# Performance work log

Hardware: AMD Instinct MI355X
Metric: run time of the kernel (lower is better)

## Reference

```python
import jax, jax.numpy as jnp
import numpy as np
import math

B, T, C = 4, 2048, 1024
N_HEAD = 16
HEAD_DIM = C // N_HEAD


def setup_inputs() -> dict:
    key = jax.random.key(0)
    k1, k2, k3, k4, k5 = jax.random.split(key, 5)
    s = 1.0 / math.sqrt(C)
    return {
        "x": jax.random.normal(k1, (B, T, C), dtype=jnp.float32),
        "W_attn": jax.random.normal(k2, (3 * C, C), dtype=jnp.float32) * s,
        "b_attn": jax.random.normal(k3, (3 * C,), dtype=jnp.float32) * 0.02,
        "W_proj": jax.random.normal(k4, (C, C), dtype=jnp.float32) * s,
        "b_proj": jax.random.normal(k5, (C,), dtype=jnp.float32) * 0.02,
    }


def reference(x, W_attn, b_attn, W_proj, b_proj):
    Bx, Tx, Cx = x.shape
    # QKV projection (torch Linear: x @ W.T + b), split into q,k,v
    qkv = jnp.einsum("btc,dc->btd", x, W_attn) + b_attn  # [B,T,3C]
    q, k, v = jnp.split(qkv, 3, axis=-1)
    # [B,T,C] -> [B,H,T,hd]
    def to_heads(t):
        return t.reshape(Bx, Tx, N_HEAD, HEAD_DIM).transpose(0, 2, 1, 3)
    q, k, v = to_heads(q), to_heads(k), to_heads(v)
    scale = 1.0 / math.sqrt(HEAD_DIM)
    att = jnp.einsum("bhqd,bhkd->bhqk", q, k) * scale  # [B,H,T,T]
    causal = jnp.tril(jnp.ones((Tx, Tx), dtype=bool))
    att = jnp.where(causal, att, -jnp.inf)
    att = jax.nn.softmax(att, axis=-1)
    y = jnp.einsum("bhqk,bhkd->bhqd", att, v)  # [B,H,T,hd]
    y = y.transpose(0, 2, 1, 3).reshape(Bx, Tx, Cx)
    y = jnp.einsum("btc,dc->btd", y, W_proj) + b_proj
    return y
```

## Files before the change

kernel.cpp:

```cpp
#include <hip/hip_runtime.h>
#include <hip/hip_bf16.h>
#include <stdint.h>

typedef unsigned short u16;
typedef __attribute__((ext_vector_type(8))) short bf16x8;
typedef __attribute__((ext_vector_type(4))) short s16x4;
typedef __attribute__((ext_vector_type(4))) float f32x4;

#define B_SZ 4
#define T_SZ 2048
#define C_SZ 1024
#define NH   16
#define HD   64
#define LOG2E 1.44269504088896340736f

__device__ __forceinline__ u16 f2bf(float f) {
  unsigned int u = __float_as_uint(f);
  u += 0x7fffu + ((u >> 16) & 1u);
  return (u16)(u >> 16);
}
__device__ __forceinline__ u16 f2bf_hu(float f) {
  return (u16)((__float_as_uint(f) + 0x8000u) >> 16);
}
__device__ __forceinline__ void gload_lds16(const u16* g, u16* l) {
  __builtin_amdgcn_global_load_lds((const __attribute__((address_space(1))) void*)g,
                                   (__attribute__((address_space(3))) void*)l, 16, 0, 0);
}

__global__ void cast3_f32_bf16(const float* __restrict__ x, const float* __restrict__ wa,
                               const float* __restrict__ wp, u16* __restrict__ xb,
                               u16* __restrict__ wab, u16* __restrict__ wpb) {
  const int n1 = 8192 * 1024 / 8, n2 = 3072 * 1024 / 8, n3 = 1024 * 1024 / 8;
  int i = blockIdx.x * blockDim.x + threadIdx.x;
  const float* in; u16* out; int idx;
  if (i < n1)            { in = x;  out = xb;  idx = i; }
  else if (i < n1 + n2)  { in = wa; out = wab; idx = i - n1; }
  else if (i < n1 + n2 + n3) { in = wp; out = wpb; idx = i - n1 - n2; }
  else return;
  const float4* p = (const float4*)in + (size_t)idx * 2;
  float4 a = p[0], b = p[1];
  bf16x8 o;
  o[0] = (short)f2bf(a.x); o[1] = (short)f2bf(a.y);
  o[2] = (short)f2bf(a.z); o[3] = (short)f2bf(a.w);
  o[4] = (short)f2bf(b.x); o[5] = (short)f2bf(b.y);
  o[6] = (short)f2bf(b.z); o[7] = (short)f2bf(b.w);
  ((bf16x8*)out)[idx] = o;
}

__launch_bounds__(512, 2)
__global__ void gemm8_qkv(const u16* __restrict__ A, const u16* __restrict__ Bw,
                          const float* __restrict__ bias,
                          u16* __restrict__ O0, u16* __restrict__ O1, u16* __restrict__ O2,
                          int M, int N, int K) {
  extern __shared__ u16 lds[];
  u16* As = lds;
  u16* Bs = lds + 32768;
  const int tid = threadIdx.x;
  const int lane = tid & 63, w = tid >> 6;
  const int wm = w >> 2, wn = w & 3;
  const int quad = lane >> 4, l16 = lane & 15;

  const int gx = gridDim.x;
  const int nwg = gx * gridDim.y;
  const int wg0 = blockIdx.y * gx + blockIdx.x;
  const int swz = (wg0 & 7) * (nwg >> 3) + (wg0 >> 3);
  const int n0 = (swz % gx) * 256;
  const int m0 = (swz / gx) * 256;

  const int dr8 = lane >> 3;
  const int dc8 = (lane & 7) ^ dr8;
  const u16* gAL = A + (size_t)(m0 + w * 8 + dr8) * K + dc8 * 8;
  const u16* gBL = Bw + (size_t)(n0 + w * 8 + dr8) * K + dc8 * 8;
  u16* dA = As + w * 512;
  u16* dB = Bs + w * 512;

  const int NT = K >> 6;

  auto stageA = [&](int tile) {
    u16* d = dA + (tile & 1) * 16384;
    const u16* g = gAL + (size_t)tile * 64;
#pragma unroll
    for (int h = 0; h < 2; ++h)
#pragma unroll
      for (int i = 0; i < 2; ++i)
        gload_lds16(g + (size_t)(h * 128 + i * 64) * K, d + h * 8192 + i * 4096);
  };
  auto stageB = [&](int tile, int h) {
    u16* d = dB + (tile & 1) * 16384 + h * 8192;
    const u16* g = gBL + (size_t)tile * 64 + (size_t)h * 128 * K;
#pragma unroll
    for (int i = 0; i < 2; ++i)
      gload_lds16(g + (size_t)i * 64 * K, d + i * 4096);
  };

  f32x4 acc[8][4];
#pragma unroll
  for (int i = 0; i < 8; i++)
#pragma unroll
    for (int j = 0; j < 4; j++) acc[i][j] = (f32x4){0.f, 0.f, 0.f, 0.f};

  stageA(0);
  stageB(0, 0); stageB(0, 1);
  stageB(1, 0); stageB(1, 1);
  asm volatile("s_waitcnt vmcnt(4)" ::: "memory");
  __builtin_amdgcn_s_barrier();

  const u16* AbaseR = As + wm * 8192;
  const u16* BbaseR = Bs + (wn >> 1) * 8192 + (wn & 1) * 64 * 64;
  const int sK0 = ((quad) ^ (l16 & 7)) * 8;
  const int sK1 = ((4 + quad) ^ (l16 & 7)) * 8;

  const int NIT = NT >> 1;
  for (int j = 0; j < NIT; ++j) {
#pragma unroll
    for (int tt = 0; tt < 2; ++tt) {
      const int tile = 2 * j + tt;
      const int bufo = (tile & 1) * 16384;
      const u16* Ab = AbaseR + bufo;
      const u16* Bb = BbaseR + bufo;
      bf16x8 bfr[4][2];
#pragma unroll
      for (int mp = 0; mp < 4; ++mp) {
        bf16x8 af[2][2];
#pragma unroll
        for (int a2 = 0; a2 < 2; ++a2) {
          const int ro = ((mp * 2 + a2) * 16 + l16) * 64;
          af[a2][0] = *(const bf16x8*)&Ab[ro + sK0];
          af[a2][1] = *(const bf16x8*)&Ab[ro + sK1];
        }
        if (mp == 0) {
#pragma unroll
          for (int nt = 0; nt < 4; ++nt) {
            const int ro = (nt * 16 + l16) * 64;
            bfr[nt][0] = *(const bf16x8*)&Bb[ro + sK0];
            bfr[nt][1] = *(const bf16x8*)&Bb[ro + sK1];
          }
        }
        if (mp == 0) { if (tile + 1 < NT) stageA(tile + 1); }
        else if (mp == 1) { if (tile + 2 < NT) stageB(tile + 2, 0); }
        else if (mp == 2) { if (tile + 2 < NT) stageB(tile + 2, 1); }
        if (mp == 0) asm volatile("s_waitcnt lgkmcnt(8)");
        asm volatile("" ::: "memory");
        __builtin_amdgcn_s_barrier();
        asm volatile("s_waitcnt lgkmcnt(0)" ::: "memory");
        __builtin_amdgcn_sched_barrier(0);
        __builtin_amdgcn_s_setprio(1);
#pragma unroll
        for (int a2 = 0; a2 < 2; ++a2)
#pragma unroll
          for (int nt = 0; nt < 4; ++nt) {
            f32x4 c = acc[mp * 2 + a2][nt];
            c = __builtin_amdgcn_mfma_f32_16x16x32_bf16(af[a2][0], bfr[nt][0], c, 0, 0, 0);
            c = __builtin_amdgcn_mfma_f32_16x16x32_bf16(af[a2][1], bfr[nt][1], c, 0, 0, 0);
            acc[mp * 2 + a2][nt] = c;
          }
        __builtin_amdgcn_s_setprio(0);
        if (mp == 3) {
          if (tile + 2 >= NT) asm volatile("s_waitcnt vmcnt(0)" ::: "memory");
          else                asm volatile("s_waitcnt vmcnt(4)" ::: "memory");
        }
        asm volatile("" ::: "memory");
        __builtin_amdgcn_s_barrier();
      }
    }
  }

  float bv[4];
#pragma unroll
  for (int nt = 0; nt < 4; nt++) bv[nt] = bias[n0 + wn * 64 + nt * 16 + l16];

  const int nsec = (n0 + wn * 64) >> 10;
  const int hh = ((n0 + wn * 64) >> 6) & 15;
  if (nsec < 2) {
    u16* dst = (nsec == 0 ? O0 : O1);
#pragma unroll
    for (int mt = 0; mt < 8; mt++) {
      const int row = m0 + wm * 128 + mt * 16 + quad * 4;
      const int bb = row >> 11;
      const int t = row & 2047;
#pragma unroll
      for (int nt = 0; nt < 4; nt++) {
        const int dh = nt * 16 + l16;
        const size_t a = (((size_t)bb * NH + hh) * T_SZ + t) * HD + dh;
#pragma unroll
        for (int r = 0; r < 4; r++)
          dst[a + (size_t)r * HD] = f2bf(acc[mt][nt][r] + bv[nt]);
      }
    }
  } else {
    u16* vth = O2;
    u16* S = lds + (size_t)w * (64 * 88);
    const int chunk = lane & 7;
#pragma unroll
    for (int hf = 0; hf < 2; ++hf) {
#pragma unroll
      for (int mt2 = 0; mt2 < 4; ++mt2) {
        const int mt = hf * 4 + mt2;
#pragma unroll
        for (int nt = 0; nt < 4; ++nt) {
          s16x4 pk;
#pragma unroll
          for (int r = 0; r < 4; ++r) pk[r] = (short)f2bf(acc[mt][nt][r] + bv[nt]);
          *(s16x4*)&S[(nt * 16 + l16) * 88 + mt2 * 16 + quad * 4] = pk;
        }
      }
      const int tbase = m0 + wm * 128 + hf * 64;
      const int bb = tbase >> 11;
      const int tb = tbase & 2047;
      const size_t vrow = ((size_t)bb * NH + hh) * HD;
#pragma unroll
      for (int i = 0; i < 8; ++i) {
        const int nr = i * 8 + (lane >> 3);
        bf16x8 vv = *(const bf16x8*)&S[nr * 88 + chunk * 8];
        *(bf16x8*)&vth[(vrow + nr) * T_SZ + tb + chunk * 8] = vv;
      }
    }
  }
}

__launch_bounds__(512, 2)
__global__ void gemm8_proj(const u16* __restrict__ A, const u16* __restrict__ Bw,
                           const float* __restrict__ bias, float* __restrict__ Cout,
                           int M, int N, int K) {
  extern __shared__ u16 lds[];
  u16* As = lds;
  u16* Bs = lds + 32768;
  const int tid = threadIdx.x;
  const int lane = tid & 63, w = tid >> 6;
  const int wm = w >> 2, wn = w & 3;
  const int quad = lane >> 4, l16 = lane & 15;

  const int gx = gridDim.x;
  const int nwg = gx * gridDim.y;
  const int wg0 = blockIdx.y * gx + blockIdx.x;
  const int swz = (wg0 & 7) * (nwg >> 3) + (wg0 >> 3);
  const int n0 = (swz % gx) * 128;
  const int m0 = (swz / gx) * 256;

  const int dr8 = lane >> 3;
  const int dc8 = (lane & 7) ^ dr8;
  const u16* gAL = A + (size_t)(m0 + w * 8 + dr8) * K + dc8 * 8;
  const u16* gBL = Bw + (size_t)(n0 + w * 8 + dr8) * K + dc8 * 8;
  u16* dA = As + w * 512;
  u16* dB = Bs + w * 512;

  const int NT = K >> 6;

  auto stageA = [&](int tile) {
    u16* d = dA + (tile & 1) * 16384;
    const u16* g = gAL + (size_t)tile * 64;
#pragma unroll
    for (int sg = 0; sg < 4; ++sg)
      gload_lds16(g + (size_t)(sg * 64) * K, d + sg * 4096);
  };
  auto stageB = [&](int tile) {
    u16* d = dB + (tile & 1) * 8192;
    const u16* g = gBL + (size_t)tile * 64;
#pragma unroll
    for (int sg = 0; sg < 2; ++sg)
      gload_lds16(g + (size_t)(sg * 64) * K, d + sg * 4096);
  };

  f32x4 acc[8][2];
#pragma unroll
  for (int i = 0; i < 8; i++)
#pragma unroll
    for (int j = 0; j < 2; j++) acc[i][j] = (f32x4){0.f, 0.f, 0.f, 0.f};

  stageA(0); stageB(0); stageB(1);
  asm volatile("s_waitcnt vmcnt(2)" ::: "memory");
  __builtin_amdgcn_s_barrier();

  const int sK0 = ((quad) ^ (l16 & 7)) * 8;
  const int sK1 = ((4 + quad) ^ (l16 & 7)) * 8;

  for (int tile = 0; tile < NT; ++tile) {
    const u16* Ab = As + (tile & 1) * 16384 + wm * 8192;
    const u16* Bb = Bs + (tile & 1) * 8192 + wn * 2048;
    bf16x8 bfr[2][2];
#pragma unroll
    for (int mp = 0; mp < 2; ++mp) {
      bf16x8 af[4][2];
#pragma unroll
      for (int a = 0; a < 4; ++a) {
        const int ro = ((mp * 4 + a) * 16 + l16) * 64;
        af[a][0] = *(const bf16x8*)&Ab[ro + sK0];
        af[a][1] = *(const bf16x8*)&Ab[ro + sK1];
      }
      if (mp == 0) {
#pragma unroll
        for (int nt = 0; nt < 2; ++nt) {
          const int ro = (nt * 16 + l16) * 64;
          bfr[nt][0] = *(const bf16x8*)&Bb[ro + sK0];
          bfr[nt][1] = *(const bf16x8*)&Bb[ro + sK1];
        }
        if (tile + 1 < NT) stageA(tile + 1);
        asm volatile("s_waitcnt lgkmcnt(8)");
      } else {
        if (tile + 2 < NT) stageB(tile + 2);
        asm volatile("s_waitcnt lgkmcnt(4)");
      }
      asm volatile("" ::: "memory");
      __builtin_amdgcn_s_barrier();
      asm volatile("s_waitcnt lgkmcnt(0)" ::: "memory");
      __builtin_amdgcn_sched_barrier(0);
      __builtin_amdgcn_s_setprio(1);
#pragma unroll
      for (int a = 0; a < 4; ++a)
#pragma unroll
        for (int nt = 0; nt < 2; ++nt) {
          f32x4 c = acc[mp * 4 + a][nt];
          c = __builtin_amdgcn_mfma_f32_16x16x32_bf16(af[a][0], bfr[nt][0], c, 0, 0, 0);
          c = __builtin_amdgcn_mfma_f32_16x16x32_bf16(af[a][1], bfr[nt][1], c, 0, 0, 0);
          acc[mp * 4 + a][nt] = c;
        }
      __builtin_amdgcn_s_setprio(0);
      if (mp == 1) {
        if (tile + 2 >= NT) asm volatile("s_waitcnt vmcnt(0)" ::: "memory");
        else                asm volatile("s_waitcnt vmcnt(2)" ::: "memory");
      }
      asm volatile("" ::: "memory");
      __builtin_amdgcn_s_barrier();
    }
  }

  float bv[2];
#pragma unroll
  for (int nt = 0; nt < 2; nt++) bv[nt] = bias[n0 + wn * 32 + nt * 16 + l16];
#pragma unroll
  for (int mt = 0; mt < 8; mt++) {
    const int row = m0 + wm * 128 + mt * 16 + quad * 4;
#pragma unroll
    for (int nt = 0; nt < 2; nt++) {
      const int col = n0 + wn * 32 + nt * 16 + l16;
#pragma unroll
      for (int r = 0; r < 4; r++)
        Cout[(size_t)(row + r) * N + col] = acc[mt][nt][r] + bv[nt];
    }
  }
}

__device__ __forceinline__ void attn_step(
    int kb, int kbn, int w, int quad, int l16, int qt128, int sw0, int sw1,
    const u16* gK0, const u16* gK1, const u16* gV0, const u16* gV1,
    u16* KsF, u16* VsF, u16* PsW,
    const bf16x8 (&qf)[2][2], f32x4 (&o)[2][4], float (&l_i)[2][4]) {
  __syncthreads();

  if (kb + 1 < kbn) {
    const int nb = (kb + 1) & 1;
    const size_t ko = (size_t)(kb + 1) * 64 * HD;
    const int vo = (kb + 1) * 64;
    gload_lds16(gK0 + ko, KsF + nb * 4096 + (2 * w) * 512);
    gload_lds16(gK1 + ko, KsF + nb * 4096 + (2 * w + 1) * 512);
    gload_lds16(gV0 + vo, VsF + nb * 4096 + (2 * w) * 512);
    gload_lds16(gV1 + vo, VsF + nb * 4096 + (2 * w + 1) * 512);
  }

  const u16* Kb = KsF + (kb & 1) * 4096;
  const u16* Vb = VsF + (kb & 1) * 4096;
  const int kt0 = kb * 64;
  const float SC = 0.125f * LOG2E;

  f32x4 s[2][4];
  __builtin_amdgcn_s_setprio(1);
#pragma unroll
  for (int nt = 0; nt < 4; nt++) {
    bf16x8 kf0 = *(const bf16x8*)&Kb[(nt * 16 + l16) * 64 + sw0];
    bf16x8 kf1 = *(const bf16x8*)&Kb[(nt * 16 + l16) * 64 + sw1];
#pragma unroll
    for (int m = 0; m < 2; m++) {
      f32x4 t0 = (f32x4){0.f, 0.f, 0.f, 0.f};
      t0 = __builtin_amdgcn_mfma_f32_16x16x32_bf16(qf[m][0], kf0, t0, 0, 0, 0);
      t0 = __builtin_amdgcn_mfma_f32_16x16x32_bf16(qf[m][1], kf1, t0, 0, 0, 0);
      s[m][nt] = t0;
    }
  }
  __builtin_amdgcn_s_setprio(0);

  bf16x8 p0a, p1a, p0b, p1b;
#pragma unroll
  for (int m = 0; m < 2; m++) {
    const int mrow = qt128 + w * 32 + m * 16;
    const int qr = mrow + quad * 4;
    const bool diag = (kt0 + 64 > mrow);

    if (diag) {
#pragma unroll
      for (int nt = 0; nt < 4; nt++) {
        const int dk = kt0 + nt * 16 + l16 - qr;
#pragma unroll
        for (int r = 0; r < 4; r++) {
          float v = (dk > r) ? -10000.f : s[m][nt][r] * SC;
          s[m][nt][r] = exp2f(v);
        }
      }
    } else {
#pragma unroll
      for (int nt = 0; nt < 4; nt++)
#pragma unroll
        for (int r = 0; r < 4; r++)
          s[m][nt][r] = exp2f(s[m][nt][r] * SC);
    }
#pragma unroll
    for (int r = 0; r < 4; r++)
      l_i[m][r] += (s[m][0][r] + s[m][1][r]) + (s[m][2][r] + s[m][3][r]);

#pragma unroll
    for (int nt = 0; nt < 4; nt++)
#pragma unroll
      for (int r = 0; r < 4; r++)
        PsW[(quad * 4 + r) * 72 + nt * 16 + l16] = f2bf_hu(s[m][nt][r]);
    if (m == 0) {
      p0a = *(const bf16x8*)&PsW[l16 * 72 + quad * 8];
      p1a = *(const bf16x8*)&PsW[l16 * 72 + 32 + quad * 8];
    } else {
      p0b = *(const bf16x8*)&PsW[l16 * 72 + quad * 8];
      p1b = *(const bf16x8*)&PsW[l16 * 72 + 32 + quad * 8];
    }
  }

  __builtin_amdgcn_s_setprio(1);
#pragma unroll
  for (int nt = 0; nt < 4; nt++) {
    bf16x8 v0 = *(const bf16x8*)&Vb[(nt * 16 + l16) * 64 + sw0];
    bf16x8 v1 = *(const bf16x8*)&Vb[(nt * 16 + l16) * 64 + sw1];
    o[0][nt] = __builtin_amdgcn_mfma_f32_16x16x32_bf16(p0a, v0, o[0][nt], 0, 0, 0);
    o[0][nt] = __builtin_amdgcn_mfma_f32_16x16x32_bf16(p1a, v1, o[0][nt], 0, 0, 0);
    o[1][nt] = __builtin_amdgcn_mfma_f32_16x16x32_bf16(p0b, v0, o[1][nt], 0, 0, 0);
    o[1][nt] = __builtin_amdgcn_mfma_f32_16x16x32_bf16(p1b, v1, o[1][nt], 0, 0, 0);
  }
  __builtin_amdgcn_s_setprio(0);
}

__launch_bounds__(256, 3)
__global__ void attn_fused(const u16* __restrict__ qh, const u16* __restrict__ kh,
                           const u16* __restrict__ vth, u16* __restrict__ out) {
  __shared__ __align__(16) u16 Ks[2][64 * 64];
  __shared__ __align__(16) u16 Vs[2][64 * 64];
  __shared__ __align__(16) u16 Ps[4][16 * 72];
  const int qt = 15 - blockIdx.z;
  const int h = blockIdx.x, b = blockIdx.y;
  const int tid = threadIdx.x;
  const int lane = tid & 63, w = tid >> 6;
  const int quad = lane >> 4, l16 = lane & 15;
  const size_t bh = (size_t)b * NH + h;
  const u16* Kbase = kh + bh * T_SZ * HD;
  const u16* Vbase = vth + bh * HD * T_SZ;
  const int qt128 = qt * 128;

  const int dr = lane >> 3;
  const int dc = (lane & 7) ^ dr;
  const u16* gK0 = Kbase + (size_t)(2 * w * 8 + dr) * HD + dc * 8;
  const u16* gK1 = Kbase + (size_t)((2 * w + 1) * 8 + dr) * HD + dc * 8;
  const u16* gV0 = Vbase + (size_t)(2 * w * 8 + dr) * T_SZ + dc * 8;
  const u16* gV1 = Vbase + (size_t)((2 * w + 1) * 8 + dr) * T_SZ + dc * 8;
  u16* KsF = &Ks[0][0];
  u16* VsF = &Vs[0][0];
  u16* PsW = &Ps[w][0];

  bf16x8 qf[2][2];
#pragma unroll
  for (int m = 0; m < 2; m++) {
    const int t = qt128 + w * 32 + m * 16 + l16;
    const u16* qrow = qh + (bh * T_SZ + t) * HD;
    qf[m][0] = *(const bf16x8*)(qrow + quad * 8);
    qf[m][1] = *(const bf16x8*)(qrow + 32 + quad * 8);
  }

  f32x4 o[2][4];
  float l_i[2][4];
#pragma unroll
  for (int m = 0; m < 2; m++)
#pragma unroll
    for (int i = 0; i < 4; i++) {
      o[m][i] = (f32x4){0.f, 0.f, 0.f, 0.f};
      l_i[m][i] = 0.f;
    }

  const int kbn = 2 * qt + 2;
  const int sw0 = (quad ^ (l16 & 7)) * 8;
  const int sw1 = ((4 + quad) ^ (l16 & 7)) * 8;

  gload_lds16(gK0, KsF + (2 * w) * 512);
  gload_lds16(gK1, KsF + (2 * w + 1) * 512);
  gload_lds16(gV0, VsF + (2 * w) * 512);
  gload_lds16(gV1, VsF + (2 * w + 1) * 512);

  for (int kb = 0; kb < kbn; kb++)
    attn_step(kb, kbn, w, quad, l16, qt128, sw0, sw1,
              gK0, gK1, gV0, gV1, KsF, VsF, PsW, qf, o, l_i);

#pragma unroll
  for (int m = 0; m < 2; m++)
#pragma unroll
    for (int r = 0; r < 4; r++) {
      float v = l_i[m][r];
      v += __shfl_xor(v, 1);
      v += __shfl_xor(v, 2);
      v += __shfl_xor(v, 4);
      v += __shfl_xor(v, 8);
      const float inv = 1.f / v;
      const int t = qt128 + w * 32 + m * 16 + quad * 4 + r;
      const size_t orow = ((size_t)b * T_SZ + t) * C_SZ + (size_t)h * HD;
#pragma unroll
      for (int nt = 0; nt < 4; nt++)
        out[orow + nt * 16 + l16] = f2bf(o[m][nt][r] * inv);
    }
}

extern "C" void kernel_launch(void* const* d_in, const int* in_sizes, int n_in,
                              void* d_out, int out_size, void* d_ws, size_t ws_size,
                              hipStream_t stream) {
  (void)in_sizes; (void)n_in; (void)out_size; (void)ws_size;
  const float* x      = (const float*)d_in[0];
  const float* W_attn = (const float*)d_in[1];
  const float* b_attn = (const float*)d_in[2];
  const float* W_proj = (const float*)d_in[3];
  const float* b_proj = (const float*)d_in[4];
  float* out = (float*)d_out;

  char* ws = (char*)d_ws;
  u16* xb  = (u16*)ws;  ws += (size_t)8192 * 1024 * 2;
  u16* Wab = (u16*)ws;  ws += (size_t)3072 * 1024 * 2;
  u16* Wpb = (u16*)ws;  ws += (size_t)1024 * 1024 * 2;
  u16* qhb = (u16*)ws;  ws += (size_t)8192 * 1024 * 2;
  u16* khb = (u16*)ws;  ws += (size_t)8192 * 1024 * 2;
  u16* vtb = (u16*)ws;  ws += (size_t)8192 * 1024 * 2;
  u16* aob = (u16*)ws;

  dim3 blk(256);
  cast3_f32_bf16<<<6144, blk, 0, stream>>>(x, W_attn, W_proj, xb, Wab, Wpb);

  gemm8_qkv<<<dim3(3072 / 256, 8192 / 256), dim3(512), 131072, stream>>>(
      xb, Wab, b_attn, qhb, khb, vtb, 8192, 3072, 1024);
  attn_fused<<<dim3(NH, B_SZ, 16), blk, 0, stream>>>(qhb, khb, vtb, aob);
  gemm8_proj<<<dim3(1024 / 128, 8192 / 256), dim3(512), 98304, stream>>>(
      aob, Wpb, b_proj, out, 8192, 1024, 1024);
}
```

Baseline: 246.5 us.

## Shrink QKV GEMM tile to 256x128 to double the workgroup count

Changes the QKV projection GEMM from 256x256 to 256x128 output tiles. The grid doubles to 768 workgroups and LDS per block drops to 96KB. The main loop, staging pipeline and V-transpose epilogue are reworked to match. The aim is better CU occupancy and wave balance, at the cost of less operand reuse per tile and more total global and LDS traffic.

```diff
diff --git a/kernel.cpp b/kernel.cpp
--- a/kernel.cpp
+++ b/kernel.cpp
@@ -48,10 +48,10 @@
 }
 
 __launch_bounds__(512, 2)
-__global__ void gemm8_qkv(const u16* __restrict__ A, const u16* __restrict__ Bw,
-                          const float* __restrict__ bias,
-                          u16* __restrict__ O0, u16* __restrict__ O1, u16* __restrict__ O2,
-                          int M, int N, int K) {
+__global__ void gemm8_qkvB(const u16* __restrict__ A, const u16* __restrict__ Bw,
+                           const float* __restrict__ bias,
+                           u16* __restrict__ O0, u16* __restrict__ O1, u16* __restrict__ O2,
+                           int M, int N, int K) {
   extern __shared__ u16 lds[];
   u16* As = lds;
   u16* Bs = lds + 32768;
@@ -64,7 +64,7 @@
   const int nwg = gx * gridDim.y;
   const int wg0 = blockIdx.y * gx + blockIdx.x;
   const int swz = (wg0 & 7) * (nwg >> 3) + (wg0 >> 3);
-  const int n0 = (swz % gx) * 256;
+  const int n0 = (swz % gx) * 128;
   const int m0 = (swz / gx) * 256;
 
   const int dr8 = lane >> 3;
@@ -80,97 +80,88 @@
     u16* d = dA + (tile & 1) * 16384;
     const u16* g = gAL + (size_t)tile * 64;
 #pragma unroll
-    for (int h = 0; h < 2; ++h)
-#pragma unroll
-      for (int i = 0; i < 2; ++i)
-        gload_lds16(g + (size_t)(h * 128 + i * 64) * K, d + h * 8192 + i * 4096);
+    for (int sg = 0; sg < 4; ++sg)
+      gload_lds16(g + (size_t)(sg * 64) * K, d + sg * 4096);
   };
-  auto stageB = [&](int tile, int h) {
-    u16* d = dB + (tile & 1) * 16384 + h * 8192;
-    const u16* g = gBL + (size_t)tile * 64 + (size_t)h * 128 * K;
-#pragma unroll
-    for (int i = 0; i < 2; ++i)
-      gload_lds16(g + (size_t)i * 64 * K, d + i * 4096);
+  auto stageB = [&](int tile) {
+    u16* d = dB + (tile & 1) * 8192;
+    const u16* g = gBL + (size_t)tile * 64;
+#pragma unroll
+    for (int sg = 0; sg < 2; ++sg)
+      gload_lds16(g + (size_t)(sg * 64) * K, d + sg * 4096);
   };
 
-  f32x4 acc[8][4];
+  f32x4 acc[8][2];
 #pragma unroll
   for (int i = 0; i < 8; i++)
 #pragma unroll
-    for (int j = 0; j < 4; j++) acc[i][j] = (f32x4){0.f, 0.f, 0.f, 0.f};
-
-  stageA(0);
-  stageB(0, 0); stageB(0, 1);
-  stageB(1, 0); stageB(1, 1);
-  asm volatile("s_waitcnt vmcnt(4)" ::: "memory");
+    for (int j = 0; j < 2; j++) acc[i][j] = (f32x4){0.f, 0.f, 0.f, 0.f};
+
+  stageA(0); stageB(0); stageB(1);
+  asm volatile("s_waitcnt vmcnt(2)" ::: "memory");
   __builtin_amdgcn_s_barrier();
 
-  const u16* AbaseR = As + wm * 8192;
-  const u16* BbaseR = Bs + (wn >> 1) * 8192 + (wn & 1) * 64 * 64;
   const int sK0 = ((quad) ^ (l16 & 7)) * 8;
   const int sK1 = ((4 + quad) ^ (l16 & 7)) * 8;
 
-  const int NIT = NT >> 1;
-  for (int j = 0; j < NIT; ++j) {
-#pragma unroll
-    for (int tt = 0; tt < 2; ++tt) {
-      const int tile = 2 * j + tt;
-      const int bufo = (tile & 1) * 16384;
-      const u16* Ab = AbaseR + bufo;
-      const u16* Bb = BbaseR + bufo;
-      bf16x8 bfr[4][2];
-#pragma unroll
-      for (int mp = 0; mp < 4; ++mp) {
-        bf16x8 af[2][2];
-#pragma unroll
-        for (int a2 = 0; a2 < 2; ++a2) {
-          const int ro = ((mp * 2 + a2) * 16 + l16) * 64;
-          af[a2][0] = *(const bf16x8*)&Ab[ro + sK0];
-          af[a2][1] = *(const bf16x8*)&Ab[ro + sK1];
+  for (int tile = 0; tile < NT; ++tile) {
+    const u16* Ab = As + (tile & 1) * 16384 + wm * 8192;
+    const u16* Bb = Bs + (tile & 1) * 8192 + wn * 2048;
+    bf16x8 bfr[2][2];
+#pragma unroll
+    for (int mp = 0; mp < 2; ++mp) {
+      bf16x8 af[4][2];
+#pragma unroll
+      for (int a = 0; a < 4; ++a) {
+        const int ro = ((mp * 4 + a) * 16 + l16) * 64;
+        af[a][0] = *(const bf16x8*)&Ab[ro + sK0];
+        af[a][1] = *(const bf16x8*)&Ab[ro + sK1];
+      }
+      if (mp == 0) {
+#pragma unroll
+        for (int nt = 0; nt < 2; ++nt) {
+          const int ro = (nt * 16 + l16) * 64;
+          bfr[nt][0] = *(const bf16x8*)&Bb[ro + sK0];
+          bfr[nt][1] = *(const bf16x8*)&Bb[ro + sK1];
         }
-        if (mp == 0) {
-#pragma unroll
-          for (int nt = 0; nt < 4; ++nt) {
-            const int ro = (nt * 16 + l16) * 64;
-            bfr[nt][0] = *(const bf16x8*)&Bb[ro + sK0];
-            bfr[nt][1] = *(const bf16x8*)&Bb[ro + sK1];
-          }
+        if (tile + 1 < NT) stageA(tile + 1);
+        asm volatile("s_waitcnt lgkmcnt(8)");
+      } else {
+        if (tile + 2 < NT) stageB(tile + 2);
+        asm volatile("s_waitcnt lgkmcnt(4)");
+      }
+      asm volatile("" ::: "memory");
+      __builtin_amdgcn_s_barrier();
+      asm volatile("s_waitcnt lgkmcnt(0)" ::: "memory");
+      __builtin_amdgcn_sched_barrier(0);
+      __builtin_amdgcn_s_setprio(1);
+#pragma unroll
+      for (int a = 0; a < 4; ++a)
+#pragma unroll
+        for (int nt = 0; nt < 2; ++nt) {
+          f32x4 c = acc[mp * 4 + a][nt];
+          c = __builtin_amdgcn_mfma_f32_16x16x32_bf16(af[a][0], bfr[nt][0], c, 0, 0, 0);
+          c = __builtin_amdgcn_mfma_f32_16x16x32_bf16(af[a][1], bfr[nt][1], c, 0, 0, 0);
+          acc[mp * 4 + a][nt] = c;
         }
-        if (mp == 0) { if (tile + 1 < NT) stageA(tile + 1); }
-        else if (mp == 1) { if (tile + 2 < NT) stageB(tile + 2, 0); }
-        else if (mp == 2) { if (tile + 2 < NT) stageB(tile + 2, 1); }
-        if (mp == 0) asm volatile("s_waitcnt lgkmcnt(8)");
-        asm volatile("" ::: "memory");
-        __builtin_amdgcn_s_barrier();
-        asm volatile("s_waitcnt lgkmcnt(0)" ::: "memory");
-        __builtin_amdgcn_sched_barrier(0);
-        __builtin_amdgcn_s_setprio(1);
-#pragma unroll
-        for (int a2 = 0; a2 < 2; ++a2)
-#pragma unroll
-          for (int nt = 0; nt < 4; ++nt) {
-            f32x4 c = acc[mp * 2 + a2][nt];
-            c = __builtin_amdgcn_mfma_f32_16x16x32_bf16(af[a2][0], bfr[nt][0], c, 0, 0, 0);
-            c = __builtin_amdgcn_mfma_f32_16x16x32_bf16(af[a2][1], bfr[nt][1], c, 0, 0, 0);
-            acc[mp * 2 + a2][nt] = c;
-          }
-        __builtin_amdgcn_s_setprio(0);
-        if (mp == 3) {
-          if (tile + 2 >= NT) asm volatile("s_waitcnt vmcnt(0)" ::: "memory");
-          else                asm volatile("s_waitcnt vmcnt(4)" ::: "memory");
-        }
-        asm volatile("" ::: "memory");
-        __builtin_amdgcn_s_barrier();
-      }
-    }
-  }
-
-  float bv[4];
-#pragma unroll
-  for (int nt = 0; nt < 4; nt++) bv[nt] = bias[n0 + wn * 64 + nt * 16 + l16];
-
-  const int nsec = (n0 + wn * 64) >> 10;
-  const int hh = ((n0 + wn * 64) >> 6) & 15;
+      __builtin_amdgcn_s_setprio(0);
+      if (mp == 1) {
+        if (tile + 2 >= NT) asm volatile("s_waitcnt vmcnt(0)" ::: "memory");
+        else                asm volatile("s_waitcnt vmcnt(2)" ::: "memory");
+      }
+      asm volatile("" ::: "memory");
+      __builtin_amdgcn_s_barrier();
+    }
+  }
+
+  float bv[2];
+#pragma unroll
+  for (int nt = 0; nt < 2; nt++) bv[nt] = bias[n0 + wn * 32 + nt * 16 + l16];
+
+  const int ncol = n0 + wn * 32;
+  const int nsec = ncol >> 10;
+  const int hh = (ncol >> 6) & 15;
+  const int dho = ncol & 63;
   if (nsec < 2) {
     u16* dst = (nsec == 0 ? O0 : O1);
 #pragma unroll
@@ -179,8 +170,8 @@
       const int bb = row >> 11;
       const int t = row & 2047;
 #pragma unroll
-      for (int nt = 0; nt < 4; nt++) {
-        const int dh = nt * 16 + l16;
+      for (int nt = 0; nt < 2; nt++) {
+        const int dh = dho + nt * 16 + l16;
         const size_t a = (((size_t)bb * NH + hh) * T_SZ + t) * HD + dh;
 #pragma unroll
         for (int r = 0; r < 4; r++)
@@ -189,31 +180,26 @@
     }
   } else {
     u16* vth = O2;
-    u16* S = lds + (size_t)w * (64 * 88);
-    const int chunk = lane & 7;
-#pragma unroll
-    for (int hf = 0; hf < 2; ++hf) {
-#pragma unroll
-      for (int mt2 = 0; mt2 < 4; ++mt2) {
-        const int mt = hf * 4 + mt2;
-#pragma unroll
-        for (int nt = 0; nt < 4; ++nt) {
-          s16x4 pk;
-#pragma unroll
-          for (int r = 0; r < 4; ++r) pk[r] = (short)f2bf(acc[mt][nt][r] + bv[nt]);
-          *(s16x4*)&S[(nt * 16 + l16) * 88 + mt2 * 16 + quad * 4] = pk;
-        }
-      }
-      const int tbase = m0 + wm * 128 + hf * 64;
-      const int bb = tbase >> 11;
-      const int tb = tbase & 2047;
-      const size_t vrow = ((size_t)bb * NH + hh) * HD;
-#pragma unroll
-      for (int i = 0; i < 8; ++i) {
-        const int nr = i * 8 + (lane >> 3);
-        bf16x8 vv = *(const bf16x8*)&S[nr * 88 + chunk * 8];
-        *(bf16x8*)&vth[(vrow + nr) * T_SZ + tb + chunk * 8] = vv;
-      }
+    u16* S = lds + (size_t)w * (32 * 136);
+#pragma unroll
+    for (int mt = 0; mt < 8; ++mt)
+#pragma unroll
+      for (int nt = 0; nt < 2; ++nt) {
+        s16x4 pk;
+#pragma unroll
+        for (int r = 0; r < 4; ++r) pk[r] = (short)f2bf(acc[mt][nt][r] + bv[nt]);
+        *(s16x4*)&S[(nt * 16 + l16) * 136 + mt * 16 + quad * 4] = pk;
+      }
+    const int tbase = m0 + wm * 128;
+    const int bb = tbase >> 11;
+    const int tb = tbase & 2047;
+    const size_t vrow = ((size_t)bb * NH + hh) * HD;
+    const int tc = (lane & 15) * 8;
+#pragma unroll
+    for (int i = 0; i < 8; ++i) {
+      const int nr = i * 4 + (lane >> 4);
+      bf16x8 vv = *(const bf16x8*)&S[nr * 136 + tc];
+      *(bf16x8*)&vth[(vrow + dho + nr) * T_SZ + tb + tc] = vv;
     }
   }
 }
@@ -532,7 +518,7 @@
   dim3 blk(256);
   cast3_f32_bf16<<<6144, blk, 0, stream>>>(x, W_attn, W_proj, xb, Wab, Wpb);
 
-  gemm8_qkv<<<dim3(3072 / 256, 8192 / 256), dim3(512), 131072, stream>>>(
+  gemm8_qkvB<<<dim3(3072 / 128, 8192 / 256), dim3(512), 98304, stream>>>(
       xb, Wab, b_attn, qhb, khb, vtb, 8192, 3072, 1024);
   attn_fused<<<dim3(NH, B_SZ, 16), blk, 0, stream>>>(qhb, khb, vtb, aob);
   gemm8_proj<<<dim3(1024 / 128, 8192 / 256), dim3(512), 98304, stream>>>(
```

After: 247.8 us. About the same (+0.5%).
